# Optimization experiments

Measured on AMD Instinct MI355X. Metric: run time of the kernel, lower is better.

The kernel has to match this reference:

```python
import jax, jax.numpy as jnp
import numpy as np


def _sign(x):
    # sign(r) = 1 if r > 0 else -1 (matches 2*(r>0)-1 in the torch code)
    return 2.0 * (x > 0).astype(x.dtype) - 1.0


def setup_inputs() -> dict:
    key = jax.random.key(0)
    k1, k2 = jax.random.split(key)
    x = jax.random.normal(k1, (32, 256, 56, 56), dtype=jnp.float32)
    weight = jax.random.normal(k2, (256, 256, 3, 3), dtype=jnp.float32)
    alpha = jnp.ones((256, 1, 1), dtype=jnp.float32)
    return {"x": x, "weight": weight, "alpha": alpha}


def reference(x, weight, alpha):
    # conv2d(sign(x), sign(W), stride=1, padding=1) * alpha
    out = jax.lax.conv_general_dilated(
        _sign(x), _sign(weight),
        window_strides=(1, 1),
        padding=[(1, 1), (1, 1)],
        dimension_numbers=("NCHW", "OIHW", "NCHW"),
    )
    return out * alpha  # alpha: (C_out, 1, 1) broadcasts over (N, C_out, H, W)
```

## Files before the change

### kernel.cpp

```cpp
#include <hip/hip_runtime.h>
#include <stdint.h>

typedef int i32x4  __attribute__((ext_vector_type(4)));
typedef int i32x16 __attribute__((ext_vector_type(16)));

#define HW     56
#define NPIX   3136
#define PADW   58
#define PPIX   3364
#define NB     32
#define CIN    256
#define COUT   256
#define STRW   32
#define ROWB   (PADW*STRW)
#define GSTR   (PPIX*STRW)
#define NSTR   (8*GSTR)
#define NKID   72

__global__ __launch_bounds__(256) void pack_x(const float* __restrict__ x,
                                              char* __restrict__ xsp) {
    int pp = blockIdx.x * 256 + threadIdx.x;
    if (pp >= PPIX) return;
    int n = blockIdx.y, g = blockIdx.z;
    int hh = pp / PADW, ww = pp % PADW;
    char* dst = xsp + (size_t)n * NSTR + (size_t)g * GSTR + (size_t)pp * STRW;
    unsigned int wd[8];
    if (hh == 0 || hh == PADW - 1 || ww == 0 || ww == PADW - 1) {
#pragma unroll
        for (int m = 0; m < 8; ++m) wd[m] = 0u;
    } else {
        const float* xp = x + ((size_t)(n * CIN + g * 32)) * NPIX
                            + (size_t)(hh - 1) * HW + (ww - 1);
#pragma unroll
        for (int m = 0; m < 8; ++m) {
            unsigned int v = 0;
#pragma unroll
            for (int jj = 0; jj < 4; ++jj) {
                unsigned int b = (xp[(size_t)(m * 4 + jj) * NPIX] > 0.0f) ? 0x01u : 0xFFu;
                v |= b << (8 * jj);
            }
            wd[m] = v;
        }
    }
    ((i32x4*)dst)[0] = *(i32x4*)&wd[0];
    ((i32x4*)dst)[1] = *(i32x4*)&wd[4];
}

__global__ __launch_bounds__(256) void pack_w(const float* __restrict__ wt,
                                              char* __restrict__ wsp) {
    int b  = blockIdx.x;
    int co = threadIdx.x;
    int g  = b / 9, r = b % 9;
    const float* wp = wt + ((size_t)co * CIN + g * 32) * 9 + r;
#pragma unroll
    for (int s = 0; s < 2; ++s) {
        unsigned int wd[4];
#pragma unroll
        for (int m = 0; m < 4; ++m) {
            unsigned int v = 0;
#pragma unroll
            for (int jj = 0; jj < 4; ++jj) {
                unsigned int bb = (wp[(size_t)(s * 16 + m * 4 + jj) * 9] > 0.0f) ? 0x01u : 0xFFu;
                v |= bb << (8 * jj);
            }
            wd[m] = v;
        }
        *(i32x4*)(wsp + ((size_t)(b * 2 + s) * COUT + co) * 16) = *(i32x4*)wd;
    }
}

__device__ inline void gload16(const void* g, void* l) {
    __builtin_amdgcn_global_load_lds(
        (const __attribute__((address_space(1))) unsigned int*)g,
        (__attribute__((address_space(3))) unsigned int*)l, 16, 0, 0);
}

__global__ __launch_bounds__(256, 2) void conv_mfma(const char* __restrict__ xsp,
                                                    const char* __restrict__ wsp,
                                                    const float* __restrict__ alpha,
                                                    float* __restrict__ out) {
    __shared__ char lA[2][4096];
    __shared__ char lB[2][4096];
    int tid   = threadIdx.x;
    int ptile = blockIdx.x;
    int mtile = blockIdx.y;
    int t7 = tid >> 7, t127 = tid & 127;

    size_t aoff = (size_t)t7 * 4096 + (size_t)(mtile * 128 + t127) * 16;
    int pix = ptile * 128 + t127;
    int n = pix / NPIX, pq = pix % NPIX;
    int h = pq / HW, w = pq % HW;
    size_t boff = (size_t)n * NSTR + (size_t)h * ROWB + (size_t)w * STRW + (size_t)t7 * 16;

    i32x16 acc[4] = {};

    gload16(wsp + aoff, &lA[0][tid * 16]);
    gload16(xsp + boff, &lB[0][tid * 16]);
    __syncthreads();

    int l = tid & 63, wv = tid >> 6;
    int s2048  = (l >> 5) * 2048;
    int l31_16 = (l & 31) * 16;

    for (int k = 0; k < NKID; ++k) {
        int buf = k & 1;
        if (k < NKID - 1) {
            int kn = k + 1;
            int g = kn / 9, r = kn % 9, kh = r / 3, kw = r % 3;
            gload16(wsp + (size_t)kn * 8192 + aoff, &lA[buf ^ 1][tid * 16]);
            gload16(xsp + boff + (size_t)g * GSTR + (size_t)kh * ROWB + (size_t)kw * STRW,
                    &lB[buf ^ 1][tid * 16]);
        }
        i32x4 bfrag = *(const i32x4*)&lB[buf][s2048 + wv * 512 + l31_16];
        i32x4 af[4];
#pragma unroll
        for (int mi = 0; mi < 4; ++mi)
            af[mi] = *(const i32x4*)&lA[buf][s2048 + mi * 512 + l31_16];
#pragma unroll
        for (int mi = 0; mi < 4; ++mi)
            acc[mi] = __builtin_amdgcn_mfma_i32_32x32x32_i8(af[mi], bfrag, acc[mi], 0, 0, 0);
        __syncthreads();
    }

    int hi = l >> 5;
    int pixo = ptile * 128 + wv * 32 + (l & 31);
    int on = pixo / NPIX, opp = pixo % NPIX;
    float* ob = out + (size_t)on * COUT * NPIX + opp;
#pragma unroll
    for (int mi = 0; mi < 4; ++mi) {
#pragma unroll
        for (int r = 0; r < 16; ++r) {
            int co = mtile * 128 + mi * 32 + (r & 3) + 8 * (r >> 2) + 4 * hi;
            ob[(size_t)co * NPIX] = alpha[co] * (float)acc[mi][r];
        }
    }
}

extern "C" void kernel_launch(void* const* d_in, const int* in_sizes, int n_in,
                              void* d_out, int out_size, void* d_ws, size_t ws_size,
                              hipStream_t stream) {
    const float* x     = (const float*)d_in[0];
    const float* wt    = (const float*)d_in[1];
    const float* alpha = (const float*)d_in[2];
    float* out = (float*)d_out;

    char* ws  = (char*)d_ws;
    char* xsp = ws;
    char* wsp = ws + (size_t)NB * NSTR;

    pack_x<<<dim3(14, NB, 8), 256, 0, stream>>>(x, xsp);
    pack_w<<<dim3(NKID), 256, 0, stream>>>(wt, wsp);
    conv_mfma<<<dim3(784, 2), 256, 0, stream>>>(xsp, wsp, alpha, out);
}
```

Before: 265.9 us.

## Double pixel tile per block and process two K-steps per barrier

The conv block now covers 256 pixels instead of 128, giving each wave a 4x2 grid of MFMA accumulators so each A fragment is reused across two B fragments. Each pipeline phase loads two K slices at once, which halves the number of __syncthreads and loop iterations. The cost is doubled accumulator registers (128 VGPRs of accumulators), a larger LDS footprint (48KB per block), and half as many blocks, which may reduce occupancy under launch_bounds(256,2).

```diff
diff --git a/kernel.cpp b/kernel.cpp
--- a/kernel.cpp
+++ b/kernel.cpp
@@ -16,6 +16,7 @@
 #define GSTR   (PPIX*STRW)
 #define NSTR   (8*GSTR)
 #define NKID   72
+#define NPH    36
 
 __global__ __launch_bounds__(256) void pack_x(const float* __restrict__ x,
                                               char* __restrict__ xsp) {
@@ -79,59 +80,89 @@
                                                     const char* __restrict__ wsp,
                                                     const float* __restrict__ alpha,
                                                     float* __restrict__ out) {
-    __shared__ char lA[2][4096];
-    __shared__ char lB[2][4096];
+    __shared__ char lA[2][8192];
+    __shared__ char lB[2][16384];
     int tid   = threadIdx.x;
     int ptile = blockIdx.x;
     int mtile = blockIdx.y;
-    int t7 = tid >> 7, t127 = tid & 127;
 
-    size_t aoff = (size_t)t7 * 4096 + (size_t)(mtile * 128 + t127) * 16;
-    int pix = ptile * 128 + t127;
+    size_t aconst = (size_t)((tid >> 7) & 1) * 4096
+                  + (size_t)(mtile * 128 + (tid & 127)) * 16;
+    int pix = ptile * 256 + tid;
     int n = pix / NPIX, pq = pix % NPIX;
     int h = pq / HW, w = pq % HW;
-    size_t boff = (size_t)n * NSTR + (size_t)h * ROWB + (size_t)w * STRW + (size_t)t7 * 16;
+    size_t boff = (size_t)n * NSTR + (size_t)h * ROWB + (size_t)w * STRW;
 
-    i32x16 acc[4] = {};
+    i32x16 acc[4][2] = {};
 
-    gload16(wsp + aoff, &lA[0][tid * 16]);
-    gload16(xsp + boff, &lB[0][tid * 16]);
+    {
+#pragma unroll
+        for (int wslot = 0; wslot < 2; ++wslot)
+            gload16(wsp + (size_t)wslot * 8192 + aconst, &lA[0][wslot * 4096 + tid * 16]);
+#pragma unroll
+        for (int wslot = 0; wslot < 4; ++wslot) {
+            int kk = wslot >> 1, s = wslot & 1;
+            gload16(xsp + boff + (size_t)kk * STRW + (size_t)s * 16,
+                    &lB[0][wslot * 4096 + tid * 16]);
+        }
+    }
     __syncthreads();
 
     int l = tid & 63, wv = tid >> 6;
-    int s2048  = (l >> 5) * 2048;
+    int sA = (l >> 5) * 2048;
+    int sB = (l >> 5) * 4096;
     int l31_16 = (l & 31) * 16;
+    int bbase = wv * 1024 + l31_16;
 
-    for (int k = 0; k < NKID; ++k) {
-        int buf = k & 1;
-        if (k < NKID - 1) {
-            int kn = k + 1;
-            int g = kn / 9, r = kn % 9, kh = r / 3, kw = r % 3;
-            gload16(wsp + (size_t)kn * 8192 + aoff, &lA[buf ^ 1][tid * 16]);
-            gload16(xsp + boff + (size_t)g * GSTR + (size_t)kh * ROWB + (size_t)kw * STRW,
-                    &lB[buf ^ 1][tid * 16]);
+    for (int t = 0; t < NPH; ++t) {
+        int buf = t & 1;
+        if (t < NPH - 1) {
+            int k0 = 2 * (t + 1);
+#pragma unroll
+            for (int wslot = 0; wslot < 2; ++wslot)
+                gload16(wsp + (size_t)(k0 + wslot) * 8192 + aconst,
+                        &lA[buf ^ 1][wslot * 4096 + tid * 16]);
+#pragma unroll
+            for (int wslot = 0; wslot < 4; ++wslot) {
+                int kidx = k0 + (wslot >> 1), s = wslot & 1;
+                int g = kidx / 9, r = kidx % 9, kh = r / 3, kw = r % 3;
+                gload16(xsp + boff + (size_t)g * GSTR + (size_t)kh * ROWB
+                            + (size_t)kw * STRW + (size_t)s * 16,
+                        &lB[buf ^ 1][wslot * 4096 + tid * 16]);
+            }
         }
-        i32x4 bfrag = *(const i32x4*)&lB[buf][s2048 + wv * 512 + l31_16];
-        i32x4 af[4];
 #pragma unroll
-        for (int mi = 0; mi < 4; ++mi)
-            af[mi] = *(const i32x4*)&lA[buf][s2048 + mi * 512 + l31_16];
+        for (int kk = 0; kk < 2; ++kk) {
+            i32x4 bf[2], af[4];
 #pragma unroll
-        for (int mi = 0; mi < 4; ++mi)
-            acc[mi] = __builtin_amdgcn_mfma_i32_32x32x32_i8(af[mi], bfrag, acc[mi], 0, 0, 0);
+            for (int ni = 0; ni < 2; ++ni)
+                bf[ni] = *(const i32x4*)&lB[buf][kk * 8192 + sB + bbase + ni * 512];
+#pragma unroll
+            for (int mi = 0; mi < 4; ++mi)
+                af[mi] = *(const i32x4*)&lA[buf][kk * 4096 + sA + mi * 512 + l31_16];
+#pragma unroll
+            for (int mi = 0; mi < 4; ++mi)
+#pragma unroll
+                for (int ni = 0; ni < 2; ++ni)
+                    acc[mi][ni] = __builtin_amdgcn_mfma_i32_32x32x32_i8(
+                        af[mi], bf[ni], acc[mi][ni], 0, 0, 0);
+        }
         __syncthreads();
     }
 
     int hi = l >> 5;
-    int pixo = ptile * 128 + wv * 32 + (l & 31);
-    int on = pixo / NPIX, opp = pixo % NPIX;
-    float* ob = out + (size_t)on * COUT * NPIX + opp;
 #pragma unroll
-    for (int mi = 0; mi < 4; ++mi) {
+    for (int ni = 0; ni < 2; ++ni) {
+        int pixo = ptile * 256 + wv * 64 + ni * 32 + (l & 31);
+        int on = pixo / NPIX, opp = pixo % NPIX;
+        float* ob = out + (size_t)on * COUT * NPIX + opp;
 #pragma unroll
-        for (int r = 0; r < 16; ++r) {
-            int co = mtile * 128 + mi * 32 + (r & 3) + 8 * (r >> 2) + 4 * hi;
-            ob[(size_t)co * NPIX] = alpha[co] * (float)acc[mi][r];
+        for (int mi = 0; mi < 4; ++mi) {
+#pragma unroll
+            for (int r = 0; r < 16; ++r) {
+                int co = mtile * 128 + mi * 32 + (r & 3) + 8 * (r >> 2) + 4 * hi;
+                ob[(size_t)co * NPIX] = alpha[co] * (float)acc[mi][ni][r];
+            }
         }
     }
 }
@@ -150,5 +181,5 @@
 
     pack_x<<<dim3(14, NB, 8), 256, 0, stream>>>(x, xsp);
     pack_w<<<dim3(NKID), 256, 0, stream>>>(wt, wsp);
-    conv_mfma<<<dim3(784, 2), 256, 0, stream>>>(xsp, wsp, alpha, out);
+    conv_mfma<<<dim3(392, 2), 256, 0, stream>>>(xsp, wsp, alpha, out);
 }
```

New measurement: 274.8 us. +3.3%, slower.
